# Performance work log

Measured on AMD Instinct MI355X. Metric: run time of the kernel, lower is better.

Reference implementation:

```python
import jax, jax.numpy as jnp
import numpy as np

KSIZE, STRIDE, H, W = 7, 4, 128, 128
NH = (H - KSIZE) // STRIDE + 1  # 31
L = NH * NH                     # 961 patches


def conv2d(x, w, b=None, stride=1):
    y = jax.lax.conv_general_dilated(x, w, (stride, stride), 'VALID',
                                     dimension_numbers=('NCHW', 'OIHW', 'NCHW'))
    if b is not None:
        y = y + b[None, :, None, None]
    return y


def refpad(x):
    return jnp.pad(x, ((0, 0), (0, 0), (1, 1), (1, 1)), mode='reflect')


def unfold(x, k, s):
    # torch.nn.Unfold equivalent, returned as (B, C, k, k, L)
    B, C, Hh, Ww = x.shape
    nh = (Hh - k) // s + 1
    nw = (Ww - k) // s + 1
    hi = (jnp.arange(nh) * s)[:, None] + jnp.arange(k)  # (nh, k)
    wi = (jnp.arange(nw) * s)[:, None] + jnp.arange(k)  # (nw, k)
    p = x[:, :, hi]            # (B, C, nh, k, W)
    p = p[:, :, :, :, wi]      # (B, C, nh, k, nw, k)
    p = p.transpose(0, 1, 3, 5, 2, 4).reshape(B, C, k, k, nh * nw)
    return p


def fold(patches, Hh, Ww, k, s):
    # patches: (B, nh, nw, C, k, k); overlap-add like torch.nn.functional.fold
    B, nh, nw, C = patches.shape[0], patches.shape[1], patches.shape[2], patches.shape[3]
    hi = (jnp.arange(nh) * s)[:, None] + jnp.arange(k)  # (nh, k)
    wi = (jnp.arange(nw) * s)[:, None] + jnp.arange(k)  # (nw, k)
    H_idx = hi[:, None, :, None]  # (nh, 1, k, 1)
    W_idx = wi[None, :, None, :]  # (1, nw, 1, k)
    vals = patches.transpose(0, 3, 1, 2, 4, 5)  # (B, C, nh, nw, k, k)
    out = jnp.zeros((B, C, Hh, Ww), patches.dtype)
    return out.at[:, :, H_idx, W_idx].add(vals)


def setup_inputs() -> dict:
    key = jax.random.key(0)
    ks = jax.random.split(key, 16)
    Cin, Ci = 32, 16            # in_channels, inter_channels
    F_in = KSIZE * KSIZE * Ci   # 784
    F_out = F_in // 4           # 196
    s = 0.05
    d = {
        'x':       jax.random.normal(ks[0], (8, Cin, H, W), jnp.float32),
        'g_w':     jax.random.normal(ks[1], (Ci, Cin, 3, 3), jnp.float32) * s,
        'g_b':     jax.random.normal(ks[2], (Ci,), jnp.float32) * s,
        'w_w':     jax.random.normal(ks[3], (Ci, Cin, 3, 3), jnp.float32) * s,
        'w_b':     jax.random.normal(ks[4], (Ci,), jnp.float32) * s,
        'theta_w': jax.random.normal(ks[5], (Cin, Ci, 1, 1), jnp.float32) * s,
        'theta_b': jax.random.normal(ks[6], (Cin,), jnp.float32) * s,
        'fc1_w':   jax.random.normal(ks[7], (F_out, F_in), jnp.float32) * s,
        'fc1_b':   jax.random.normal(ks[8], (F_out,), jnp.float32) * s,
        'mconv_w': jax.random.normal(ks[9], (L, L), jnp.float32) * s,
        'mconv_b': jax.random.normal(ks[10], (L,), jnp.float32) * s,
        'mfc_w':   jax.random.normal(ks[11], (L, L), jnp.float32) * s,
        'mfc_b':   jax.random.normal(ks[12], (L,), jnp.float32) * s,
        'c1_w':    jax.random.normal(ks[13], (Cin // 2, Cin, 3, 3), jnp.float32) * s,
        'c2_w':    jax.random.normal(ks[14], (Cin, Cin // 2, 1, 1), jnp.float32) * s,
    }
    return d


def reference(x, g_w, g_b, w_w, w_b, theta_w, theta_b, fc1_w, fc1_b,
              mconv_w, mconv_b, mfc_w, mfc_b, c1_w, c2_w):
    residual = x
    x1 = conv2d(refpad(x), g_w, g_b)        # (B, Ci, H, W)
    x2 = conv2d(refpad(x), w_w, w_b)        # (B, Ci, H, W)
    x3 = conv2d(x1, theta_w, theta_b)       # (B, Cin, H, W)
    B = x.shape[0]
    Cin = x.shape[1]

    p6 = unfold(x1, KSIZE, STRIDE).transpose(0, 4, 1, 2, 3).reshape(B, L, -1)   # (B,L,Ci*49)
    p4 = unfold(x2, KSIZE, STRIDE).transpose(0, 4, 1, 2, 3).reshape(B, L, -1)   # (B,L,Ci*49)
    p62 = unfold(x3, KSIZE, STRIDE).transpose(0, 4, 1, 2, 3).reshape(B, L, -1)  # (B,L,Cin*49)

    wf = p4 @ fc1_w.T + fc1_b   # (B, L, F)
    xf = p6 @ fc1_w.T + fc1_b   # (B, L, F)
    A = jnp.einsum('blf,bmf->blm', wf, xf)  # (B, L, L)

    # Ti1 (Conv1d k=1 over patch dim) + Ti2 (Linear over patch dim, transposed)
    Ti = jnp.einsum('nc,bcm->bnm', mconv_w + mfc_w, A) + (mconv_b + mfc_b)[None, :, None]
    mask = jax.nn.sigmoid(Ti)
    mask_b = (mask != 0.0).astype(A.dtype)

    scale = wf.shape[-1] ** -0.5
    Am = jax.nn.softmax(A * mask * scale, axis=-1) * mask_b  # (B, L, L)

    y = jnp.einsum('blm,bmf->blf', Am, p62)  # (B, L, Cin*49)
    y = y.reshape(B, NH, NH, Cin, KSIZE, KSIZE)
    out = fold(y, H, W, KSIZE, STRIDE)       # (B, Cin, H, W)

    # BasicBlock: conv3x3(reflect) -> lrelu -> conv1x1 -> lrelu
    o = jax.nn.leaky_relu(conv2d(refpad(out), c1_w), 0.2)
    o = jax.nn.leaky_relu(conv2d(o, c2_w), 0.2)
    out = residual + o
    return Am, out
```

## Files before the change

### kernel.cpp

```cpp
#include <hip/hip_runtime.h>
#include <math.h>

namespace {
constexpr int Bn   = 8;
constexpr int CIN  = 32;
constexpr int CI   = 16;
constexpr int Lp   = 961;
constexpr int FIN  = 784;
constexpr int FOUT = 196;
constexpr int F62  = 1568;

constexpr int FCP  = 224;
constexpr long long FCB = 961LL * FCP;
constexpr int KP   = 992;
constexpr long long WFTB = 196LL * KP;
constexpr long long AMBB = 961LL * KP;
constexpr long long PBTB = 1568LL * KP;
constexpr long long AB   = 961LL * 961;
constexpr int YLD  = 964;
constexpr long long YB = 1568LL * YLD;
constexpr int CK   = 288;
}

typedef __attribute__((ext_vector_type(8))) short short8x;
typedef __attribute__((ext_vector_type(4))) float floatx4;
typedef __attribute__((ext_vector_type(4))) unsigned short ushort4x;

static __device__ __forceinline__ unsigned short f2bf(float x) {
    unsigned int u = __builtin_bit_cast(unsigned int, x);
    u += 0x7fffu + ((u >> 16) & 1u);
    return (unsigned short)(u >> 16);
}
static __device__ __forceinline__ float bf2f(unsigned short h) {
    return __builtin_bit_cast(float, ((unsigned int)h) << 16);
}

__global__ __launch_bounds__(256)
void prep_k(const float* __restrict__ g_w, const float* __restrict__ w_w,
            const float* __restrict__ c1_w,
            unsigned short* __restrict__ cwh, unsigned short* __restrict__ cwl,
            unsigned short* __restrict__ c1h, unsigned short* __restrict__ c1l,
            const float* __restrict__ mconv_w, const float* __restrict__ mfc_w,
            unsigned short* __restrict__ Mwh, unsigned short* __restrict__ Mwl,
            const float* __restrict__ mconv_b, const float* __restrict__ mfc_b,
            float* __restrict__ Mb,
            const float* __restrict__ fc1w,
            unsigned short* __restrict__ Wh, unsigned short* __restrict__ Wl,
            unsigned short* __restrict__ wfTh, unsigned short* __restrict__ wfTl)
{
    int i = blockIdx.x * 256 + threadIdx.x;
    if (i < 9216) {
        int n = i / CK, k = i - n * CK;
        int t = k >> 5, ci = k & 31;
        float v = (n < 16) ? g_w[n * 288 + ci * 9 + t]
                           : w_w[(n - 16) * 288 + ci * 9 + t];
        unsigned short h = f2bf(v);
        cwh[i] = h; cwl[i] = f2bf(v - bf2f(h));
    } else if (i < 13824) {
        int k2 = i - 9216;
        int n = k2 / CK, k = k2 - n * CK;
        int t = k >> 5, ci = k & 31;
        float v = c1_w[n * 288 + ci * 9 + t];
        unsigned short h = f2bf(v);
        c1h[k2] = h; c1l[k2] = f2bf(v - bf2f(h));
    } else if (i < 967136) {
        int k = i - 13824;
        int n = k / KP, c = k - n * KP;
        float v = (c < 961) ? (mconv_w[n * 961 + c] + mfc_w[n * 961 + c]) : 0.0f;
        unsigned short h = f2bf(v);
        Mwh[k] = h; Mwl[k] = f2bf(v - bf2f(h));
    } else if (i < 968097) {
        int k = i - 967136;
        Mb[k] = mconv_b[k] + mfc_b[k];
    } else if (i < 1172897) {
        int k = i - 968097;
        int n = k / 800, kk = k - n * 800;
        int tap = kk >> 4, c = kk & 15;
        float v = (n < 196 && tap < 49) ? fc1w[n * 784 + c * 49 + tap] : 0.0f;
        unsigned short h = f2bf(v);
        Wh[k] = h; Wl[k] = f2bf(v - bf2f(h));
    } else if (i < 1223073) {
        int k = i - 1172897;
        int row = k >> 5, c = k & 31;
        long long pos = (long long)row * KP + 960 + c;
        wfTh[pos] = 0; wfTl[pos] = 0;
    }
}

__global__ __launch_bounds__(256)
void cls_k(const float* __restrict__ src,
           unsigned short* __restrict__ dh_, unsigned short* __restrict__ dl_)
{
    __shared__ float T[4096];
    const int b = blockIdx.x & 7, h = blockIdx.x >> 3;
    const float* sb = src + (size_t)b * 32 * 16384 + h * 128;
    for (int i = threadIdx.x; i < 4096; i += 256) {
        int ci = i >> 7, w = i & 127;
        T[i] = sb[ci * 16384 + w];
    }
    __syncthreads();
    long long obase = ((long long)b * 16384 + (long long)h * 128) * 32;
    for (int i = threadIdx.x; i < 512; i += 256) {
        int w = i >> 2, o = i & 3;
        unsigned short hv[8], lv[8];
        #pragma unroll
        for (int e = 0; e < 8; ++e) {
            float v = T[(o * 8 + e) * 128 + w];
            unsigned short hh = f2bf(v);
            hv[e] = hh; lv[e] = f2bf(v - bf2f(hh));
        }
        *(short8x*)(dh_ + obase + w * 32 + o * 8) = *(short8x*)hv;
        *(short8x*)(dl_ + obase + w * 32 + o * 8) = *(short8x*)lv;
    }
}

template<int NOUT, bool BIAS, bool LEAKY, bool CLOUT>
__global__ __launch_bounds__(256)
void convcl_k(const unsigned short* __restrict__ Ih,
              const unsigned short* __restrict__ Il,
              const unsigned short* __restrict__ Bh,
              const unsigned short* __restrict__ Bl,
              const float* __restrict__ b1, const float* __restrict__ b2,
              float* __restrict__ o1,
              unsigned short* __restrict__ o1h, unsigned short* __restrict__ o1l,
              unsigned short* __restrict__ o2h, unsigned short* __restrict__ o2l)
{
    __shared__ unsigned short IsH[12480];
    __shared__ unsigned short IsL[12480];

    const int tid = threadIdx.x;
    const int b   = blockIdx.x & 7;
    const int h   = blockIdx.x >> 3;

    for (int i = tid; i < 1560; i += 256) {
        int p = i >> 2, o = i & 3;
        int dh = (p >= 260) ? 2 : (p >= 130) ? 1 : 0;
        int c  = p - dh * 130;
        int gh = h - 1 + dh; gh = (gh < 0) ? 1 : (gh > 127 ? 126 : gh);
        int gw = c - 1;      gw = (gw < 0) ? 1 : (gw > 127 ? 126 : gw);
        long long src = (((long long)b * 16384 + gh * 128 + gw) << 5) + o * 8;
        int dst = p * 32 + ((o ^ ((c >> 1) & 3)) << 3);
        *(short8x*)&IsH[dst] = *(const short8x*)(Ih + src);
        *(short8x*)&IsL[dst] = *(const short8x*)(Il + src);
    }
    __syncthreads();

    const int lane = tid & 63;
    const int wv   = tid >> 6;
    const int wm   = wv * 32;
    const int fr   = lane & 15;
    const int kq   = lane >> 4;
    constexpr int NF = NOUT / 16;

    floatx4 acc[2][NF];
    #pragma unroll
    for (int i = 0; i < 2; ++i)
        #pragma unroll
        for (int j = 0; j < NF; ++j)
            acc[i][j] = (floatx4){0.f, 0.f, 0.f, 0.f};

    #pragma unroll
    for (int t = 0; t < 9; ++t) {
        const int dh = t / 3, dw = t % 3;
        short8x bh_[NF], bl_[NF];
        #pragma unroll
        for (int j = 0; j < NF; ++j) {
            int nr = j * 16 + fr;
            bh_[j] = *(const short8x*)(Bh + nr * CK + t * 32 + kq * 8);
            bl_[j] = *(const short8x*)(Bl + nr * CK + t * 32 + kq * 8);
        }
        #pragma unroll
        for (int i = 0; i < 2; ++i) {
            int col = wm + i * 16 + fr + dw;
            int off = (dh * 130 + col) * 32 + ((kq ^ ((col >> 1) & 3)) << 3);
            short8x ah = *(const short8x*)&IsH[off];
            short8x al = *(const short8x*)&IsL[off];
            #pragma unroll
            for (int j = 0; j < NF; ++j) {
                acc[i][j] = __builtin_amdgcn_mfma_f32_16x16x32_bf16(ah, bh_[j], acc[i][j], 0, 0, 0);
                acc[i][j] = __builtin_amdgcn_mfma_f32_16x16x32_bf16(ah, bl_[j], acc[i][j], 0, 0, 0);
                acc[i][j] = __builtin_amdgcn_mfma_f32_16x16x32_bf16(al, bh_[j], acc[i][j], 0, 0, 0);
            }
        }
    }

    if constexpr (CLOUT) {
        __syncthreads();
        #pragma unroll
        for (int j = 0; j < NF; ++j) {
            int n = j * 16 + fr;
            float bnv = 0.0f;
            if constexpr (BIAS) bnv = (n < 16) ? b1[n] : b2[n - 16];
            #pragma unroll
            for (int i = 0; i < 2; ++i) {
                int pb = wm + i * 16 + kq * 4;
                #pragma unroll
                for (int r = 0; r < 4; ++r) {
                    float v = acc[i][j][r] + bnv;
                    if constexpr (LEAKY) v = (v >= 0.0f) ? v : 0.2f * v;
                    unsigned short hh = f2bf(v);
                    IsH[(pb + r) * 32 + n] = hh;
                    IsL[(pb + r) * 32 + n] = f2bf(v - bf2f(hh));
                }
            }
        }
        __syncthreads();
        const int p  = tid >> 1;
        const int c0 = (tid & 1) * 8;
        long long base = ((long long)b * 16384 + (long long)h * 128 + p) * 16 + c0;
        *(short8x*)(o1h + base) = *(short8x*)&IsH[p * 32 + c0];
        *(short8x*)(o1l + base) = *(short8x*)&IsL[p * 32 + c0];
        if constexpr (NOUT == 32) {
            *(short8x*)(o2h + base) = *(short8x*)&IsH[p * 32 + 16 + c0];
            *(short8x*)(o2l + base) = *(short8x*)&IsL[p * 32 + 16 + c0];
        }
    } else {
        #pragma unroll
        for (int j = 0; j < NF; ++j) {
            int n = j * 16 + fr;
            float bnv = 0.0f;
            if constexpr (BIAS) bnv = (n < 16) ? b1[n] : b2[n - 16];
            float* dst = o1 + (((size_t)b * NOUT + n) * 128 + h) * 128;
            #pragma unroll
            for (int i = 0; i < 2; ++i) {
                int wb = wm + i * 16 + kq * 4;
                floatx4 ov;
                #pragma unroll
                for (int r = 0; r < 4; ++r) {
                    float v = acc[i][j][r] + bnv;
                    if constexpr (LEAKY) v = (v >= 0.0f) ? v : 0.2f * v;
                    ov[r] = v;
                }
                *(floatx4*)(dst + wb) = ov;
            }
        }
    }
}

template<bool CLSRC, bool BIAS, bool LEAKY, bool RESID>
__global__ __launch_bounds__(256)
void conv1x1p_k(const float* __restrict__ src,
                const unsigned short* __restrict__ srcH,
                const unsigned short* __restrict__ srcL,
                const float* __restrict__ wgt,
                const float* __restrict__ bias, const float* __restrict__ resid,
                float* __restrict__ out)
{
    int idx = blockIdx.x * 256 + threadIdx.x;
    int pix = idx & 16383;
    int b   = idx >> 14;
    float s[16];
    if constexpr (CLSRC) {
        long long base = ((long long)b * 16384 + pix) * 16;
        short8x h0 = *(const short8x*)(srcH + base);
        short8x h1 = *(const short8x*)(srcH + base + 8);
        short8x l0 = *(const short8x*)(srcL + base);
        short8x l1 = *(const short8x*)(srcL + base + 8);
        #pragma unroll
        for (int ci = 0; ci < 8; ++ci) {
            s[ci]     = bf2f((unsigned short)h0[ci]) + bf2f((unsigned short)l0[ci]);
            s[ci + 8] = bf2f((unsigned short)h1[ci]) + bf2f((unsigned short)l1[ci]);
        }
    } else {
        const float* sb = src + (size_t)b * CI * 16384 + pix;
        #pragma unroll
        for (int ci = 0; ci < CI; ++ci) s[ci] = sb[ci * 16384];
    }
    size_t ob = (size_t)b * 32 * 16384 + pix;
    #pragma unroll
    for (int co = 0; co < 32; ++co) {
        const float* wrow = wgt + co * CI;
        float acc = BIAS ? bias[co] : 0.0f;
        #pragma unroll
        for (int ci = 0; ci < CI; ++ci) acc += wrow[ci] * s[ci];
        if constexpr (LEAKY) acc = (acc >= 0.0f) ? acc : 0.2f * acc;
        if constexpr (RESID) acc += resid[ob + (size_t)co * 16384];
        out[ob + (size_t)co * 16384] = acc;
    }
}

__global__ __launch_bounds__(256)
void fcmfma2_k(const unsigned short* __restrict__ x1h,
               const unsigned short* __restrict__ x1l,
               const unsigned short* __restrict__ x2h,
               const unsigned short* __restrict__ x2l,
               const unsigned short* __restrict__ Wh,
               const unsigned short* __restrict__ Wl,
               const float* __restrict__ bias,
               unsigned short* __restrict__ Xfh, unsigned short* __restrict__ Xfl,
               unsigned short* __restrict__ Wfh, unsigned short* __restrict__ Wfl,
               unsigned short* __restrict__ DTh, unsigned short* __restrict__ DTl)
{
    __shared__ unsigned short AsH[64*32], AsL[64*32], BsH[64*32], BsL[64*32];
    const int tid = threadIdx.x;
    const bool wrt = blockIdx.x >= 484;
    const int bid = wrt ? (int)blockIdx.x - 484 : (int)blockIdx.x;
    const unsigned short* Ah = wrt ? x2h : x1h;
    const unsigned short* Al = wrt ? x2l : x1l;
    unsigned short* Dh = wrt ? Wfh : Xfh;
    unsigned short* Dl = wrt ? Wfl : Xfl;
    const int tm0 = (bid >> 2) * 64;
    const int tn0 = (bid & 3) * 64;

    const int lr = tid >> 2;
    const int lc = tid & 3;
    const int gm = tm0 + lr;
    const bool mok = gm < 7688;
    int gb16 = 0;
    if (mok) {
        int b = gm / 961, pi = gm - b * 961;
        int ih = pi / 31, iw = pi - ih * 31;
        gb16 = (b * 16384 + ih * 512 + iw * 4) * 16;
    }
    const int tapAdd = lc >> 1;
    const int c0a    = (lc & 1) * 8;
    const int pc = ((lc ^ ((lr >> 1) & 3))) * 8;
    const unsigned short* Whr = Wh + (tn0 + lr) * 800;
    const unsigned short* Wlr = Wl + (tn0 + lr) * 800;

    const int lane = tid & 63, wv = tid >> 6;
    const int wm = (wv >> 1) * 32, wn = (wv & 1) * 32;
    const int fr = lane & 15, kq = lane >> 4;

    floatx4 acc[2][2];
    #pragma unroll
    for (int i = 0; i < 2; ++i)
        #pragma unroll
        for (int j = 0; j < 2; ++j)
            acc[i][j] = (floatx4){0.f, 0.f, 0.f, 0.f};

    const short8x zz = {0,0,0,0,0,0,0,0};
    short8x pah, pal, pwh, pwl;
    auto loadA = [&](int k0) {
        int tap = (k0 >> 4) + tapAdd;
        if (mok && tap < 49) {
            int kh = tap / 7, kw = tap - kh * 7;
            int off = gb16 + kh * 2048 + kw * 16 + c0a;
            pah = *(const short8x*)(Ah + off);
            pal = *(const short8x*)(Al + off);
        } else { pah = zz; pal = zz; }
    };
    auto loadW = [&](int k0) {
        pwh = *(const short8x*)(Whr + k0 + lc * 8);
        pwl = *(const short8x*)(Wlr + k0 + lc * 8);
    };

    loadA(0); loadW(0);
    for (int k0 = 0; k0 < 800; k0 += 32) {
        *(short8x*)&AsH[lr * 32 + pc] = pah;
        *(short8x*)&AsL[lr * 32 + pc] = pal;
        *(short8x*)&BsH[lr * 32 + pc] = pwh;
        *(short8x*)&BsL[lr * 32 + pc] = pwl;
        __syncthreads();
        if (k0 + 32 < 800) { loadA(k0 + 32); loadW(k0 + 32); }
        short8x ah[2], al[2], bh[2], bl[2];
        #pragma unroll
        for (int i = 0; i < 2; ++i) {
            int mr = wm + i * 16 + fr;
            int off = mr * 32 + ((kq ^ ((mr >> 1) & 3)) * 8);
            ah[i] = *(const short8x*)&AsH[off];
            al[i] = *(const short8x*)&AsL[off];
        }
        #pragma unroll
        for (int j = 0; j < 2; ++j) {
            int nr = wn + j * 16 + fr;
            int off = nr * 32 + ((kq ^ ((nr >> 1) & 3)) * 8);
            bh[j] = *(const short8x*)&BsH[off];
            bl[j] = *(const short8x*)&BsL[off];
        }
        #pragma unroll
        for (int i = 0; i < 2; ++i)
            #pragma unroll
            for (int j = 0; j < 2; ++j) {
                acc[i][j] = __builtin_amdgcn_mfma_f32_16x16x32_bf16(ah[i], bh[j], acc[i][j], 0, 0, 0);
                acc[i][j] = __builtin_amdgcn_mfma_f32_16x16x32_bf16(ah[i], bl[j], acc[i][j], 0, 0, 0);
                acc[i][j] = __builtin_amdgcn_mfma_f32_16x16x32_bf16(al[i], bh[j], acc[i][j], 0, 0, 0);
            }
        __syncthreads();
    }

    #pragma unroll
    for (int j = 0; j < 2; ++j) {
        int n = tn0 + wn + j * 16 + fr;
        if (n >= FCP) continue;
        float bn = (n < 196) ? bias[n] : 0.0f;
        #pragma unroll
        for (int i = 0; i < 2; ++i) {
            #pragma unroll
            for (int r = 0; r < 4; ++r) {
                int l = tm0 + wm + i * 16 + kq * 4 + r;
                if (l >= 7688) continue;
                int b = l / 961, pi = l - b * 961;
                float v = (n < 196) ? (acc[i][j][r] + bn) : 0.0f;
                unsigned short h = f2bf(v);
                unsigned short lo = f2bf(v - bf2f(h));
                long long base = (long long)b * FCB + (long long)pi * FCP + n;
                Dh[base] = h;
                Dl[base] = lo;
                if (wrt && n < 196) {
                    long long tb = (long long)b * WFTB + (long long)n * KP + pi;
                    DTh[tb] = h;
                    DTl[tb] = lo;
                }
            }
        }
    }
}

__global__ __launch_bounds__(256)
void w2mfma_k(const unsigned short* __restrict__ Xhi,
              const unsigned short* __restrict__ Xlo,
              const unsigned short* __restrict__ Yhi,
              const unsigned short* __restrict__ Ylo,
              unsigned short* __restrict__ W2h,
              unsigned short* __restrict__ W2l)
{
    __shared__ unsigned short XsH[4096], XsL[4096], YsH[4096], YsL[4096];
    const int b   = blockIdx.x & 7;
    const int t   = blockIdx.x >> 3;
    const int tm0 = (t >> 1) * 128;
    const int tn0 = (t & 1) * 128;
    const unsigned short* Ybh = Yhi + (long long)b * WFTB;
    const unsigned short* Ybl = Ylo + (long long)b * WFTB;
    const int tid = threadIdx.x;

    const int sr  = tid >> 1;
    const int sc0 = (tid & 1) * 2;
    const bool xok = (tm0 + sr) < 961;
    const bool yok = (tn0 + sr) < 196;
    const unsigned short* Xrh = Xhi + (long long)(tm0 + sr) * KP;
    const unsigned short* Xrl = Xlo + (long long)(tm0 + sr) * KP;
    const unsigned short* Yrh = Ybh + (long long)(tn0 + sr) * KP;
    const unsigned short* Yrl = Ybl + (long long)(tn0 + sr) * KP;
    const int swz = (sr >> 1) & 3;

    const int lane = tid & 63;
    const int wv   = tid >> 6;
    const int wm   = (wv >> 1) * 64, wn = (wv & 1) * 64;
    const int fr   = lane & 15;
    const int kq   = lane >> 4;

    floatx4 acc[4][4];
    #pragma unroll
    for (int i = 0; i < 4; ++i)
        #pragma unroll
        for (int j = 0; j < 4; ++j)
            acc[i][j] = (floatx4){0.f, 0.f, 0.f, 0.f};

    const short8x zz = {0,0,0,0,0,0,0,0};
    short8x pxh[2], pxl[2], pyh[2], pyl[2];
    auto loadK = [&](int k0) {
        #pragma unroll
        for (int c = 0; c < 2; ++c) {
            int kc = sc0 + c;
            pxh[c] = xok ? *(const short8x*)(Xrh + k0 + kc * 8) : zz;
            pxl[c] = xok ? *(const short8x*)(Xrl + k0 + kc * 8) : zz;
            pyh[c] = yok ? *(const short8x*)(Yrh + k0 + kc * 8) : zz;
            pyl[c] = yok ? *(const short8x*)(Yrl + k0 + kc * 8) : zz;
        }
    };

    loadK(0);
    for (int k0 = 0; k0 < KP; k0 += 32) {
        #pragma unroll
        for (int c = 0; c < 2; ++c) {
            int pc = (sc0 + c) ^ swz;
            *(short8x*)&XsH[sr * 32 + pc * 8] = pxh[c];
            *(short8x*)&XsL[sr * 32 + pc * 8] = pxl[c];
            *(short8x*)&YsH[sr * 32 + pc * 8] = pyh[c];
            *(short8x*)&YsL[sr * 32 + pc * 8] = pyl[c];
        }
        __syncthreads();
        if (k0 + 32 < KP) loadK(k0 + 32);
        short8x bh[4], bl[4];
        #pragma unroll
        for (int j = 0; j < 4; ++j) {
            int nr = wn + j * 16 + fr;
            int off = nr * 32 + ((kq ^ ((nr >> 1) & 3)) * 8);
            bh[j] = *(const short8x*)&YsH[off];
            bl[j] = *(const short8x*)&YsL[off];
        }
        #pragma unroll
        for (int i = 0; i < 4; ++i) {
            int mr = wm + i * 16 + fr;
            int off = mr * 32 + ((kq ^ ((mr >> 1) & 3)) * 8);
            short8x ah = *(const short8x*)&XsH[off];
            short8x al = *(const short8x*)&XsL[off];
            #pragma unroll
            for (int j = 0; j < 4; ++j) {
                acc[i][j] = __builtin_amdgcn_mfma_f32_16x16x32_bf16(ah, bh[j], acc[i][j], 0, 0, 0);
                acc[i][j] = __builtin_amdgcn_mfma_f32_16x16x32_bf16(ah, bl[j], acc[i][j], 0, 0, 0);
                acc[i][j] = __builtin_amdgcn_mfma_f32_16x16x32_bf16(al, bh[j], acc[i][j], 0, 0, 0);
            }
        }
        __syncthreads();
    }

    unsigned short* Wh2 = W2h + (long long)b * FCB;
    unsigned short* Wl2 = W2l + (long long)b * FCB;
    #pragma unroll
    for (int j = 0; j < 4; ++j) {
        int f = tn0 + wn + j * 16 + fr;
        if (f >= FCP) continue;
        #pragma unroll
        for (int i = 0; i < 4; ++i) {
            int lb = tm0 + wm + i * 16 + kq * 4;
            #pragma unroll
            for (int r = 0; r < 4; ++r) {
                int l = lb + r;
                if (l >= 961) continue;
                float v = acc[i][j][r];
                unsigned short h = f2bf(v);
                long long pos = (long long)l * FCP + f;
                Wh2[pos] = h;
                Wl2[pos] = f2bf(v - bf2f(h));
            }
        }
    }
}

__global__ __launch_bounds__(256, 2)
void atimfma_k(const unsigned short* __restrict__ Wfh,
               const unsigned short* __restrict__ Wfl,
               const unsigned short* __restrict__ W2h,
               const unsigned short* __restrict__ W2l,
               const unsigned short* __restrict__ Xfh,
               const unsigned short* __restrict__ Xfl,
               const float* __restrict__ Mb,
               float* __restrict__ Sout)
{
    const int b   = blockIdx.x & 7;
    const int t   = blockIdx.x >> 3;
    const int tm0 = (t >> 3) * 128;
    const int tn0 = (t & 7) * 128;
    const int tid = threadIdx.x;

    const int lane = tid & 63;
    const int wv   = tid >> 6;
    const int wm   = (wv >> 1) * 64, wn = (wv & 1) * 64;
    const int fr   = lane & 15;
    const int kq   = lane >> 4;

    const long long bb = (long long)b * FCB;
    const unsigned short* A1h = Wfh + bb;
    const unsigned short* A1l = Wfl + bb;
    const unsigned short* A2h = W2h + bb;
    const unsigned short* A2l = W2l + bb;
    const unsigned short* Byh = Xfh + bb;
    const unsigned short* Byl = Xfl + bb;

    int aoff[4], boff[4];
    #pragma unroll
    for (int i = 0; i < 4; ++i) {
        int r = tm0 + wm + i * 16 + fr; if (r > 960) r = 960;
        aoff[i] = r * FCP + kq * 8;
    }
    #pragma unroll
    for (int j = 0; j < 4; ++j) {
        int r = tn0 + wn + j * 16 + fr; if (r > 960) r = 960;
        boff[j] = r * FCP + kq * 8;
    }

    floatx4 accA[4][4], accT[4][4];
    #pragma unroll
    for (int i = 0; i < 4; ++i)
        #pragma unroll
        for (int j = 0; j < 4; ++j) {
            accA[i][j] = (floatx4){0.f, 0.f, 0.f, 0.f};
            accT[i][j] = (floatx4){0.f, 0.f, 0.f, 0.f};
        }

    short8x f1h[2][4], f1l[2][4], f2h[2][4], f2l[2][4], fbh[2][4], fbl[2][4];

    #pragma unroll
    for (int j = 0; j < 4; ++j) {
        fbh[0][j] = *(const short8x*)(Byh + boff[j]);
        fbl[0][j] = *(const short8x*)(Byl + boff[j]);
    }
    #pragma unroll
    for (int i = 0; i < 4; ++i) {
        f1h[0][i] = *(const short8x*)(A1h + aoff[i]);
        f1l[0][i] = *(const short8x*)(A1l + aoff[i]);
        f2h[0][i] = *(const short8x*)(A2h + aoff[i]);
        f2l[0][i] = *(const short8x*)(A2l + aoff[i]);
    }

    #pragma unroll
    for (int ks = 0; ks < 7; ++ks) {
        const int cur = ks & 1, nxt = cur ^ 1;
        if (ks < 6) {
            const int k0 = (ks + 1) * 32;
            #pragma unroll
            for (int j = 0; j < 4; ++j) {
                fbh[nxt][j] = *(const short8x*)(Byh + boff[j] + k0);
                fbl[nxt][j] = *(const short8x*)(Byl + boff[j] + k0);
            }
            #pragma unroll
            for (int i = 0; i < 4; ++i) {
                f1h[nxt][i] = *(const short8x*)(A1h + aoff[i] + k0);
                f1l[nxt][i] = *(const short8x*)(A1l + aoff[i] + k0);
                f2h[nxt][i] = *(const short8x*)(A2h + aoff[i] + k0);
                f2l[nxt][i] = *(const short8x*)(A2l + aoff[i] + k0);
            }
        }
        #pragma unroll
        for (int i = 0; i < 4; ++i) {
            #pragma unroll
            for (int j = 0; j < 4; ++j) {
                accA[i][j] = __builtin_amdgcn_mfma_f32_16x16x32_bf16(f1h[cur][i], fbh[cur][j], accA[i][j], 0, 0, 0);
                accA[i][j] = __builtin_amdgcn_mfma_f32_16x16x32_bf16(f1h[cur][i], fbl[cur][j], accA[i][j], 0, 0, 0);
                accA[i][j] = __builtin_amdgcn_mfma_f32_16x16x32_bf16(f1l[cur][i], fbh[cur][j], accA[i][j], 0, 0, 0);
                accT[i][j] = __builtin_amdgcn_mfma_f32_16x16x32_bf16(f2h[cur][i], fbh[cur][j], accT[i][j], 0, 0, 0);
                accT[i][j] = __builtin_amdgcn_mfma_f32_16x16x32_bf16(f2h[cur][i], fbl[cur][j], accT[i][j], 0, 0, 0);
                accT[i][j] = __builtin_amdgcn_mfma_f32_16x16x32_bf16(f2l[cur][i], fbh[cur][j], accT[i][j], 0, 0, 0);
            }
        }
    }

    const float scale = 0.07142857142857142f;
    float* Sb = Sout + (long long)b * AB;
    #pragma unroll
    for (int j = 0; j < 4; ++j) {
        int m = tn0 + wn + j * 16 + fr;
        if (m >= 961) continue;
        #pragma unroll
        for (int i = 0; i < 4; ++i) {
            int lb = tm0 + wm + i * 16 + kq * 4;
            #pragma unroll
            for (int r = 0; r < 4; ++r) {
                int l = lb + r;
                if (l >= 961) continue;
                float ti = accT[i][j][r] + Mb[l];
                float mask = 1.0f / (1.0f + expf(-ti));
                Sb[(long long)l * 961 + m] = accA[i][j][r] * mask * scale;
            }
        }
    }
}

__global__ __launch_bounds__(256)
void softmax_mask_k(const float* __restrict__ S, float* __restrict__ Am,
                    unsigned short* __restrict__ Amb)
{
    int row = blockIdx.x;
    const float* srow = S + (long long)row * Lp;
    float*       orow = Am + (long long)row * Lp;
    unsigned short* brow = Amb + (long long)row * KP;
    int tid = threadIdx.x;

    float s[4], mb[4];
    float lmax = -INFINITY;
    #pragma unroll
    for (int j = 0; j < 4; ++j) {
        int m = tid + j * 256;
        if (m < Lp) {
            float v = srow[m];
            s[j]  = v;
            mb[j] = (v != 0.0f) ? 1.0f : 0.0f;
            lmax  = fmaxf(lmax, v);
        } else { s[j] = -INFINITY; mb[j] = 0.0f; }
    }
    __shared__ float red[256];
    red[tid] = lmax; __syncthreads();
    #pragma unroll
    for (int off = 128; off > 0; off >>= 1) {
        if (tid < off) red[tid] = fmaxf(red[tid], red[tid + off]);
        __syncthreads();
    }
    float rmax = red[0];
    __syncthreads();

    float e[4];
    float lsum = 0.0f;
    #pragma unroll
    for (int j = 0; j < 4; ++j) {
        int m = tid + j * 256;
        e[j] = (m < Lp) ? expf(s[j] - rmax) : 0.0f;
        lsum += e[j];
    }
    red[tid] = lsum; __syncthreads();
    #pragma unroll
    for (int off = 128; off > 0; off >>= 1) {
        if (tid < off) red[tid] += red[tid + off];
        __syncthreads();
    }
    float inv = 1.0f / red[0];
    #pragma unroll
    for (int j = 0; j < 4; ++j) {
        int m = tid + j * 256;
        if (m < Lp) {
            float v = e[j] * inv * mb[j];
            orow[m] = v;
            brow[m] = f2bf(v);
        } else if (m < KP) {
            brow[m] = 0;
        }
    }
}

__global__ __launch_bounds__(256)
void p62bt_k(const float* __restrict__ x3, unsigned short* __restrict__ out)
{
    int idx = blockIdx.x * 256 + threadIdx.x;
    if (idx >= 8 * 1568 * 124) return;
    int ck = idx % 124;
    int t  = idx / 124;
    int n  = t % 1568;
    int b  = t / 1568;
    int c = n / 49, rr = n - c * 49;
    int kh = rr / 7, kw = rr - kh * 7;
    const float* src = x3 + (long long)b * 524288 + c * 16384 + kh * 128 + kw;
    int k = ck * 8;
    unsigned short v[8];
    #pragma unroll
    for (int j = 0; j < 8; ++j) {
        int kk = k + j;
        if (kk < Lp) {
            int ih = kk / 31, iw = kk - ih * 31;
            v[j] = f2bf(src[ih * 512 + iw * 4]);
        } else v[j] = 0;
    }
    *(short8x*)(out + ((long long)b * 1568 + n) * KP + k) = *(short8x*)v;
}

__global__ __launch_bounds__(256)
void ymfma_k(const unsigned short* __restrict__ Amb,
             const unsigned short* __restrict__ Pbt,
             unsigned short* __restrict__ yT)
{
    __shared__ unsigned short As[128 * 32];
    __shared__ unsigned short Bs[128 * 32];
    const int b   = blockIdx.x & 7;
    const int t   = blockIdx.x >> 3;
    const int tn0 = (t % 13) * 128;
    const int tm0 = (t / 13) * 128;
    const unsigned short* Ab = Amb + (long long)b * AMBB;
    const unsigned short* Bb = Pbt + (long long)b * PBTB;
    const int tid = threadIdx.x;

    const int sr  = tid >> 1;
    const int sc0 = (tid & 1) * 2;
    const bool aok = (tm0 + sr) < Lp;
    const bool bok = (tn0 + sr) < F62;
    const unsigned short* Arow = Ab + (long long)(tm0 + sr) * KP;
    const unsigned short* Brow = Bb + (long long)(tn0 + sr) * KP;
    const int swz = (sr >> 1) & 3;

    const int lane = tid & 63;
    const int wv   = tid >> 6;
    const int wm   = (wv >> 1) * 64, wn = (wv & 1) * 64;
    const int fr   = lane & 15;
    const int kq   = lane >> 4;

    floatx4 acc[4][4];
    #pragma unroll
    for (int i = 0; i < 4; ++i)
        #pragma unroll
        for (int j = 0; j < 4; ++j)
            acc[i][j] = (floatx4){0.f, 0.f, 0.f, 0.f};

    const short8x zz = {0,0,0,0,0,0,0,0};
    short8x pa[2], pb[2];
    auto loadK = [&](int k0) {
        #pragma unroll
        for (int c = 0; c < 2; ++c) {
            int kc = sc0 + c;
            pa[c] = aok ? *(const short8x*)(Arow + k0 + kc * 8) : zz;
            pb[c] = bok ? *(const short8x*)(Brow + k0 + kc * 8) : zz;
        }
    };

    loadK(0);
    for (int k0 = 0; k0 < Lp; k0 += 32) {
        #pragma unroll
        for (int c = 0; c < 2; ++c) {
            int pc = (sc0 + c) ^ swz;
            *(short8x*)&As[sr * 32 + pc * 8] = pa[c];
            *(short8x*)&Bs[sr * 32 + pc * 8] = pb[c];
        }
        __syncthreads();
        if (k0 + 32 < Lp) loadK(k0 + 32);
        short8x af[4], bfr[4];
        #pragma unroll
        for (int i = 0; i < 4; ++i) {
            int mr = wm + i * 16 + fr;
            af[i] = *(const short8x*)&As[mr * 32 + ((kq ^ ((mr >> 1) & 3)) * 8)];
        }
        #pragma unroll
        for (int j = 0; j < 4; ++j) {
            int nr = wn + j * 16 + fr;
            bfr[j] = *(const short8x*)&Bs[nr * 32 + ((kq ^ ((nr >> 1) & 3)) * 8)];
        }
        #pragma unroll
        for (int i = 0; i < 4; ++i)
            #pragma unroll
            for (int j = 0; j < 4; ++j)
                acc[i][j] = __builtin_amdgcn_mfma_f32_16x16x32_bf16(
                                af[i], bfr[j], acc[i][j], 0, 0, 0);
        __syncthreads();
    }

    unsigned short* Yb = yT + (long long)b * YB;
    #pragma unroll
    for (int j = 0; j < 4; ++j) {
        int n = tn0 + wn + j * 16 + fr;
        if (n >= F62) continue;
        unsigned short* Yr = Yb + (long long)n * YLD;
        #pragma unroll
        for (int i = 0; i < 4; ++i) {
            int lb = tm0 + wm + i * 16 + kq * 4;
            if (lb >= Lp) continue;
            ushort4x hv;
            #pragma unroll
            for (int r = 0; r < 4; ++r) hv[r] = f2bf(acc[i][j][r]);
            if (lb + 3 < Lp) {
                *(ushort4x*)(Yr + lb) = hv;
            } else {
                #pragma unroll
                for (int r = 0; r < 4; ++r)
                    if (lb + r < Lp) Yr[lb + r] = hv[r];
            }
        }
    }
}

__global__ __launch_bounds__(256)
void foldg_k(const unsigned short* __restrict__ yT, float* __restrict__ out)
{
    int idx = blockIdx.x * 256 + threadIdx.x;
    int wc = idx & 127;
    int hr = (idx >> 7) & 127;
    int c  = (idx >> 14) & 31;
    int b  = idx >> 19;
    int ih_lo = (hr >= 6) ? ((hr - 3) >> 2) : 0;
    int ih_hi = min(hr >> 2, 30);
    int iw_lo = (wc >= 6) ? ((wc - 3) >> 2) : 0;
    int iw_hi = min(wc >> 2, 30);
    const unsigned short* Yb = yT + (long long)b * YB + (long long)c * 49 * YLD;
    float acc = 0.0f;
    for (int ih = ih_lo; ih <= ih_hi; ++ih) {
        int kh = hr - 4 * ih;
        for (int iw = iw_lo; iw <= iw_hi; ++iw) {
            int kw = wc - 4 * iw;
            acc += bf2f(Yb[(kh * 7 + kw) * YLD + ih * 31 + iw]);
        }
    }
    out[idx] = acc;
}

extern "C" void kernel_launch(void* const* d_in, const int* in_sizes, int n_in,
                              void* d_out, int out_size, void* d_ws, size_t ws_size,
                              hipStream_t stream)
{
    const float* x       = (const float*)d_in[0];
    const float* g_w     = (const float*)d_in[1];
    const float* g_b     = (const float*)d_in[2];
    const float* w_w     = (const float*)d_in[3];
    const float* w_b     = (const float*)d_in[4];
    const float* theta_w = (const float*)d_in[5];
    const float* theta_b = (const float*)d_in[6];
    const float* fc1_w   = (const float*)d_in[7];
    const float* fc1_b   = (const float*)d_in[8];
    const float* mconv_w = (const float*)d_in[9];
    const float* mconv_b = (const float*)d_in[10];
    const float* mfc_w   = (const float*)d_in[11];
    const float* mfc_b   = (const float*)d_in[12];
    const float* c1_w    = (const float*)d_in[13];
    const float* c2_w    = (const float*)d_in[14];

    float* Am_out    = (float*)d_out;
    float* final_out = Am_out + (size_t)Bn * Lp * Lp;

    float* ws = (float*)d_ws;
    unsigned short* x1clH = (unsigned short*)ws;
    unsigned short* x1clL = (unsigned short*)(ws + 1048576);
    unsigned short* x2clH = (unsigned short*)(ws + 2097152);
    unsigned short* x2clL = (unsigned short*)(ws + 3145728);
    float* x1f   = ws;
    float* x3    = ws + 4194304;
    unsigned short* xf_hi = (unsigned short*)(ws + 8388608);
    unsigned short* xf_lo = (unsigned short*)(ws + 9249664);
    unsigned short* wf_hi = (unsigned short*)(ws + 10110720);
    unsigned short* wf_lo = (unsigned short*)(ws + 10971776);
    float* Abuf  = ws + 11832832;
    unsigned short* wfT_hi = (unsigned short*)(ws + 19221000);
    unsigned short* wfT_lo = (unsigned short*)(ws + 19998728);
    unsigned short* W2_hi  = (unsigned short*)(ws + 20776456);
    unsigned short* W2_lo  = (unsigned short*)(ws + 21637512);
    unsigned short* Mw_hi = (unsigned short*)(ws + 26847496);
    unsigned short* Mw_lo = (unsigned short*)(ws + 27324152);
    float* Mb    = ws + 27800808;
    unsigned short* fc1wh = (unsigned short*)(ws + 27801832);
    unsigned short* fc1wl = (unsigned short*)(ws + 27904232);
    unsigned short* cwh = (unsigned short*)(ws + 4194304);
    unsigned short* cwl = cwh + 16384;
    unsigned short* c1h = (unsigned short*)(ws + 28006632);
    unsigned short* c1l = c1h + 8192;
    unsigned short* xclH = (unsigned short*)(ws + 11832832);
    unsigned short* xclL = (unsigned short*)(ws + 13929984);
    unsigned short* Am_bf16 = (unsigned short*)ws;
    unsigned short* p62bT   = (unsigned short*)Abuf;
    unsigned short* yT      = wfT_hi;
    unsigned short* fclH    = xclH;
    unsigned short* fclL    = xclL;

    prep_k<<<4778, 256, 0, stream>>>(
        g_w, w_w, c1_w, cwh, cwl, c1h, c1l,
        mconv_w, mfc_w, Mw_hi, Mw_lo,
        mconv_b, mfc_b, Mb, fc1_w, fc1wh, fc1wl,
        wfT_hi, wfT_lo);

    cls_k<<<1024, 256, 0, stream>>>(x, xclH, xclL);

    convcl_k<32, true, false, true><<<1024, 256, 0, stream>>>(
        xclH, xclL, cwh, cwl, g_b, w_b,
        nullptr, x1clH, x1clL, x2clH, x2clL);

    conv1x1p_k<true, true, false, false><<<512, 256, 0, stream>>>(
        nullptr, x1clH, x1clL, theta_w, theta_b, nullptr, x3);

    fcmfma2_k<<<968, 256, 0, stream>>>(
        x1clH, x1clL, x2clH, x2clL, fc1wh, fc1wl, fc1_b,
        xf_hi, xf_lo, wf_hi, wf_lo, wfT_hi, wfT_lo);

    w2mfma_k<<<128, 256, 0, stream>>>(
        Mw_hi, Mw_lo, wfT_hi, wfT_lo, W2_hi, W2_lo);

    atimfma_k<<<512, 256, 0, stream>>>(
        wf_hi, wf_lo, W2_hi, W2_lo, xf_hi, xf_lo, Mb, Abuf);

    softmax_mask_k<<<7688, 256, 0, stream>>>(Abuf, Am_out, Am_bf16);

    p62bt_k<<<6077, 256, 0, stream>>>(x3, p62bT);

    ymfma_k<<<832, 256, 0, stream>>>(Am_bf16, p62bT, yT);

    foldg_k<<<16384, 256, 0, stream>>>(yT, x3);

    cls_k<<<1024, 256, 0, stream>>>(x3, fclH, fclL);

    convcl_k<16, false, true, false><<<1024, 256, 0, stream>>>(
        fclH, fclL, c1h, c1l, nullptr, nullptr,
        x1f, nullptr, nullptr, nullptr, nullptr);

    conv1x1p_k<false, false, true, true><<<512, 256, 0, stream>>>(
        x1f, nullptr, nullptr, c2_w, nullptr, x, final_out);
}
```

Baseline: 459.4 us.

## Split-K the W2 GEMM and merge softmax with p62 transpose launch

```diff
diff --git a/kernel.cpp b/kernel.cpp
--- a/kernel.cpp
+++ b/kernel.cpp
@@ -408,16 +408,17 @@
 }
 
 __global__ __launch_bounds__(256)
-void w2mfma_k(const unsigned short* __restrict__ Xhi,
-              const unsigned short* __restrict__ Xlo,
-              const unsigned short* __restrict__ Yhi,
-              const unsigned short* __restrict__ Ylo,
-              unsigned short* __restrict__ W2h,
-              unsigned short* __restrict__ W2l)
+void w2split_k(const unsigned short* __restrict__ Xhi,
+               const unsigned short* __restrict__ Xlo,
+               const unsigned short* __restrict__ Yhi,
+               const unsigned short* __restrict__ Ylo,
+               float* __restrict__ Part)
 {
     __shared__ unsigned short XsH[4096], XsL[4096], YsH[4096], YsL[4096];
-    const int b   = blockIdx.x & 7;
-    const int t   = blockIdx.x >> 3;
+    const int sk  = blockIdx.x >> 7;
+    const int rem = blockIdx.x & 127;
+    const int b   = rem & 7;
+    const int t   = rem >> 3;
     const int tm0 = (t >> 1) * 128;
     const int tn0 = (t & 1) * 128;
     const unsigned short* Ybh = Yhi + (long long)b * WFTB;
@@ -460,8 +461,10 @@
         }
     };
 
-    loadK(0);
-    for (int k0 = 0; k0 < KP; k0 += 32) {
+    const int kb = sk * 256;
+    const int ke = (kb + 256 < KP) ? kb + 256 : KP;
+    loadK(kb);
+    for (int k0 = kb; k0 < ke; k0 += 32) {
         #pragma unroll
         for (int c = 0; c < 2; ++c) {
             int pc = (sc0 + c) ^ swz;
@@ -471,7 +474,7 @@
             *(short8x*)&YsL[sr * 32 + pc * 8] = pyl[c];
         }
         __syncthreads();
-        if (k0 + 32 < KP) loadK(k0 + 32);
+        if (k0 + 32 < ke) loadK(k0 + 32);
         short8x bh[4], bl[4];
         #pragma unroll
         for (int j = 0; j < 4; ++j) {
@@ -496,8 +499,7 @@
         __syncthreads();
     }
 
-    unsigned short* Wh2 = W2h + (long long)b * FCB;
-    unsigned short* Wl2 = W2l + (long long)b * FCB;
+    float* Pb = Part + ((long long)(sk * 8 + b) * 961) * FCP;
     #pragma unroll
     for (int j = 0; j < 4; ++j) {
         int f = tn0 + wn + j * 16 + fr;
@@ -509,14 +511,38 @@
             for (int r = 0; r < 4; ++r) {
                 int l = lb + r;
                 if (l >= 961) continue;
-                float v = acc[i][j][r];
-                unsigned short h = f2bf(v);
-                long long pos = (long long)l * FCP + f;
-                Wh2[pos] = h;
-                Wl2[pos] = f2bf(v - bf2f(h));
-            }
-        }
-    }
+                Pb[(long long)l * FCP + f] = acc[i][j][r];
+            }
+        }
+    }
+}
+
+__global__ __launch_bounds__(256)
+void w2comb_k(const float* __restrict__ P,
+              unsigned short* __restrict__ W2h,
+              unsigned short* __restrict__ W2l)
+{
+    int idx = blockIdx.x * 256 + threadIdx.x;
+    if (idx >= 430592) return;
+    int f4 = idx % 56;
+    int t  = idx / 56;
+    int l  = t % 961;
+    int b  = t / 961;
+    long long off = ((long long)b * 961 + l) * FCP + f4 * 4;
+    const long long cs = 8LL * 961 * FCP;
+    floatx4 s = *(const floatx4*)(P + off)
+              + *(const floatx4*)(P + off + cs)
+              + *(const floatx4*)(P + off + 2 * cs)
+              + *(const floatx4*)(P + off + 3 * cs);
+    ushort4x hv, lv;
+    #pragma unroll
+    for (int r = 0; r < 4; ++r) {
+        unsigned short h = f2bf(s[r]);
+        hv[r] = h; lv[r] = f2bf(s[r] - bf2f(h));
+    }
+    long long pos = (long long)b * FCB + (long long)l * FCP + f4 * 4;
+    *(ushort4x*)(W2h + pos) = hv;
+    *(ushort4x*)(W2l + pos) = lv;
 }
 
 __global__ __launch_bounds__(256, 2)
@@ -639,88 +665,87 @@
 }
 
 __global__ __launch_bounds__(256)
-void softmax_mask_k(const float* __restrict__ S, float* __restrict__ Am,
-                    unsigned short* __restrict__ Amb)
-{
-    int row = blockIdx.x;
-    const float* srow = S + (long long)row * Lp;
-    float*       orow = Am + (long long)row * Lp;
-    unsigned short* brow = Amb + (long long)row * KP;
-    int tid = threadIdx.x;
-
-    float s[4], mb[4];
-    float lmax = -INFINITY;
-    #pragma unroll
-    for (int j = 0; j < 4; ++j) {
-        int m = tid + j * 256;
-        if (m < Lp) {
-            float v = srow[m];
-            s[j]  = v;
-            mb[j] = (v != 0.0f) ? 1.0f : 0.0f;
-            lmax  = fmaxf(lmax, v);
-        } else { s[j] = -INFINITY; mb[j] = 0.0f; }
-    }
-    __shared__ float red[256];
-    red[tid] = lmax; __syncthreads();
-    #pragma unroll
-    for (int off = 128; off > 0; off >>= 1) {
-        if (tid < off) red[tid] = fmaxf(red[tid], red[tid + off]);
+void smp62_k(const float* __restrict__ S, float* __restrict__ Am,
+             unsigned short* __restrict__ Amb,
+             const float* __restrict__ x3, unsigned short* __restrict__ pout)
+{
+    if (blockIdx.x < 7688) {
+        int row = blockIdx.x;
+        const float* srow = S + (long long)row * Lp;
+        float*       orow = Am + (long long)row * Lp;
+        unsigned short* brow = Amb + (long long)row * KP;
+        int tid = threadIdx.x;
+
+        float s[4], mb[4];
+        float lmax = -INFINITY;
+        #pragma unroll
+        for (int j = 0; j < 4; ++j) {
+            int m = tid + j * 256;
+            if (m < Lp) {
+                float v = srow[m];
+                s[j]  = v;
+                mb[j] = (v != 0.0f) ? 1.0f : 0.0f;
+                lmax  = fmaxf(lmax, v);
+            } else { s[j] = -INFINITY; mb[j] = 0.0f; }
+        }
+        __shared__ float red[256];
+        red[tid] = lmax; __syncthreads();
+        #pragma unroll
+        for (int off = 128; off > 0; off >>= 1) {
+            if (tid < off) red[tid] = fmaxf(red[tid], red[tid + off]);
+            __syncthreads();
+        }
+        float rmax = red[0];
         __syncthreads();
-    }
-    float rmax = red[0];
-    __syncthreads();
-
-    float e[4];
-    float lsum = 0.0f;
-    #pragma unroll
-    for (int j = 0; j < 4; ++j) {
-        int m = tid + j * 256;
-        e[j] = (m < Lp) ? expf(s[j] - rmax) : 0.0f;
-        lsum += e[j];
-    }
-    red[tid] = lsum; __syncthreads();
-    #pragma unroll
-    for (int off = 128; off > 0; off >>= 1) {
-        if (tid < off) red[tid] += red[tid + off];
-        __syncthreads();
-    }
-    float inv = 1.0f / red[0];
-    #pragma unroll
-    for (int j = 0; j < 4; ++j) {
-        int m = tid + j * 256;
-        if (m < Lp) {
-            float v = e[j] * inv * mb[j];
-            orow[m] = v;
-            brow[m] = f2bf(v);
-        } else if (m < KP) {
-            brow[m] = 0;
-        }
-    }
-}
-
-__global__ __launch_bounds__(256)
-void p62bt_k(const float* __restrict__ x3, unsigned short* __restrict__ out)
-{
-    int idx = blockIdx.x * 256 + threadIdx.x;
-    if (idx >= 8 * 1568 * 124) return;
-    int ck = idx % 124;
-    int t  = idx / 124;
-    int n  = t % 1568;
-    int b  = t / 1568;
-    int c = n / 49, rr = n - c * 49;
-    int kh = rr / 7, kw = rr - kh * 7;
-    const float* src = x3 + (long long)b * 524288 + c * 16384 + kh * 128 + kw;
-    int k = ck * 8;
-    unsigned short v[8];
-    #pragma unroll
-    for (int j = 0; j < 8; ++j) {
-        int kk = k + j;
-        if (kk < Lp) {
-            int ih = kk / 31, iw = kk - ih * 31;
-            v[j] = f2bf(src[ih * 512 + iw * 4]);
-        } else v[j] = 0;
-    }
-    *(short8x*)(out + ((long long)b * 1568 + n) * KP + k) = *(short8x*)v;
+
+        float e[4];
+        float lsum = 0.0f;
+        #pragma unroll
+        for (int j = 0; j < 4; ++j) {
+            int m = tid + j * 256;
+            e[j] = (m < Lp) ? expf(s[j] - rmax) : 0.0f;
+            lsum += e[j];
+        }
+        red[tid] = lsum; __syncthreads();
+        #pragma unroll
+        for (int off = 128; off > 0; off >>= 1) {
+            if (tid < off) red[tid] += red[tid + off];
+            __syncthreads();
+        }
+        float inv = 1.0f / red[0];
+        #pragma unroll
+        for (int j = 0; j < 4; ++j) {
+            int m = tid + j * 256;
+            if (m < Lp) {
+                float v = e[j] * inv * mb[j];
+                orow[m] = v;
+                brow[m] = f2bf(v);
+            } else if (m < KP) {
+                brow[m] = 0;
+            }
+        }
+    } else {
+        int idx = ((int)blockIdx.x - 7688) * 256 + threadIdx.x;
+        if (idx >= 8 * 1568 * 124) return;
+        int ck = idx % 124;
+        int t  = idx / 124;
+        int n  = t % 1568;
+        int b  = t / 1568;
+        int c = n / 49, rr = n - c * 49;
+        int kh = rr / 7, kw = rr - kh * 7;
+        const float* src = x3 + (long long)b * 524288 + c * 16384 + kh * 128 + kw;
+        int k = ck * 8;
+        unsigned short v[8];
+        #pragma unroll
+        for (int j = 0; j < 8; ++j) {
+            int kk = k + j;
+            if (kk < Lp) {
+                int ih = kk / 31, iw = kk - ih * 31;
+                v[j] = f2bf(src[ih * 512 + iw * 4]);
+            } else v[j] = 0;
+        }
+        *(short8x*)(pout + ((long long)b * 1568 + n) * KP + k) = *(short8x*)v;
+    }
 }
 
 __global__ __launch_bounds__(256)
@@ -898,11 +923,12 @@
     unsigned short* c1l = c1h + 8192;
     unsigned short* xclH = (unsigned short*)(ws + 11832832);
     unsigned short* xclL = (unsigned short*)(ws + 13929984);
+    float* w2part = Abuf;
     unsigned short* Am_bf16 = (unsigned short*)ws;
-    unsigned short* p62bT   = (unsigned short*)Abuf;
-    unsigned short* yT      = wfT_hi;
-    unsigned short* fclH    = xclH;
-    unsigned short* fclL    = xclL;
+    unsigned short* p62bT = (unsigned short*)(ws + 19221000);
+    unsigned short* yT    = (unsigned short*)Abuf;
+    unsigned short* fclH  = xclH;
+    unsigned short* fclL  = xclL;
 
     prep_k<<<4778, 256, 0, stream>>>(
         g_w, w_w, c1_w, cwh, cwl, c1h, c1l,
@@ -923,15 +949,15 @@
         x1clH, x1clL, x2clH, x2clL, fc1wh, fc1wl, fc1_b,
         xf_hi, xf_lo, wf_hi, wf_lo, wfT_hi, wfT_lo);
 
-    w2mfma_k<<<128, 256, 0, stream>>>(
-        Mw_hi, Mw_lo, wfT_hi, wfT_lo, W2_hi, W2_lo);
+    w2split_k<<<512, 256, 0, stream>>>(
+        Mw_hi, Mw_lo, wfT_hi, wfT_lo, w2part);
+    w2comb_k<<<1682, 256, 0, stream>>>(w2part, W2_hi, W2_lo);
 
     atimfma_k<<<512, 256, 0, stream>>>(
         wf_hi, wf_lo, W2_hi, W2_lo, xf_hi, xf_lo, Mb, Abuf);
 
-    softmax_mask_k<<<7688, 256, 0, stream>>>(Abuf, Am_out, Am_bf16);
-
-    p62bt_k<<<6077, 256, 0, stream>>>(x3, p62bT);
+    smp62_k<<<13765, 256, 0, stream>>>(
+        Abuf, Am_out, Am_bf16, x3, p62bT);
 
     ymfma_k<<<832, 256, 0, stream>>>(Am_bf16, p62bT, yT);
 
```

New measurement: 460.3 us. About the same (+0.2%).
